# Optimization experiments

Hardware: AMD Instinct MI355X
Metric: run time of the kernel (lower is better)

## Reference

```python
import jax, jax.numpy as jnp
import numpy as np

B, S, D, H = 2, 2048, 1024, 16
HD = D // H  # head dim 64
LN_EPS = 1e-12


def setup_inputs() -> dict:
    key = jax.random.key(0)
    ks = jax.random.split(key, 10)
    sc = 0.02
    return {
        "input_tensor": jax.random.normal(ks[0], (B, S, D), dtype=jnp.float32),
        "attention_mask": jnp.zeros((B, 1, 1, S), dtype=jnp.float32),
        "Wq": jax.random.normal(ks[1], (D, D), dtype=jnp.float32) * sc,
        "bq": jnp.zeros((D,), dtype=jnp.float32),
        "Wk": jax.random.normal(ks[2], (D, D), dtype=jnp.float32) * sc,
        "bk": jnp.zeros((D,), dtype=jnp.float32),
        "Wv": jax.random.normal(ks[3], (D, D), dtype=jnp.float32) * sc,
        "bv": jnp.zeros((D,), dtype=jnp.float32),
        "Wo": jax.random.normal(ks[4], (D, D), dtype=jnp.float32) * sc,
        "bo": jnp.zeros((D,), dtype=jnp.float32),
        "ln_gamma": jnp.ones((D,), dtype=jnp.float32),
        "ln_beta": jnp.zeros((D,), dtype=jnp.float32),
    }


def _split_heads(x):
    # [B,S,D] -> [B,H,S,hd]
    return x.reshape(B, S, H, HD).transpose(0, 2, 1, 3)


def reference(input_tensor, attention_mask, Wq, bq, Wk, bk, Wv, bv, Wo, bo, ln_gamma, ln_beta):
    q = _split_heads(input_tensor @ Wq + bq)
    k = _split_heads(input_tensor @ Wk + bk)
    v = _split_heads(input_tensor @ Wv + bv)
    scores = jnp.einsum("bhqd,bhkd->bhqk", q, k) / jnp.sqrt(jnp.float32(HD))
    scores = scores + attention_mask  # additive mask broadcast
    probs = jax.nn.softmax(scores, axis=-1)
    ctx = jnp.einsum("bhqk,bhkd->bhqd", probs, v)
    ctx = ctx.transpose(0, 2, 1, 3).reshape(B, S, D)
    hidden = ctx @ Wo + bo
    x = hidden + input_tensor
    mu = jnp.mean(x, axis=-1, keepdims=True)
    var = jnp.mean(jnp.square(x - mu), axis=-1, keepdims=True)
    return (x - mu) / jnp.sqrt(var + LN_EPS) * ln_gamma + ln_beta
```

## Files before the change

kernel.cpp:

```cpp
#include <hip/hip_runtime.h>
#include <stdint.h>

#define Bb 2
#define Ss 2048
#define Dd 1024
#define Hh 16
#define HD 64
#define Mtot 4096

typedef __bf16 bf16x8 __attribute__((ext_vector_type(8)));
typedef float f32x4 __attribute__((ext_vector_type(4)));
typedef unsigned short ushort_t;

#if __has_builtin(__builtin_amdgcn_exp2f)
#define EXP2(x) __builtin_amdgcn_exp2f(x)
#else
#define EXP2(x) __expf((x) * 0.6931472f)
#endif

__device__ __forceinline__ float bf2f(ushort_t u) {
    union { uint32_t i; float f; } v;
    v.i = ((uint32_t)u) << 16;
    return v.f;
}

__device__ __forceinline__ ushort_t f2bf(float f) {
    union { float f; uint32_t i; } v;
    v.f = f;
    uint32_t u = v.i;
    u += 0x7FFFu + ((u >> 16) & 1u);
    return (ushort_t)(u >> 16);
}

__device__ __forceinline__ uint32_t fbits(float f) {
    union { float f; uint32_t i; } v; v.f = f; return v.i;
}

__device__ __forceinline__ float load_in(const void* p, size_t i, int isf32) {
    if (isf32) return ((const float*)p)[i];
    return bf2f(((const ushort_t*)p)[i]);
}

__device__ __forceinline__ void gload_lds16(const void* g, void* l) {
    __builtin_amdgcn_global_load_lds(
        (const __attribute__((address_space(1))) void*)g,
        (__attribute__((address_space(3))) void*)l, 16, 0, 0);
}

#define NVEC 525568ull
__global__ __launch_bounds__(256) void prep_k(
    const void* X, const void* mask, const void* bq, const void* bk,
    const void* bv, const void* bo, const void* g, const void* be,
    const void* Wq, const void* Wk, const void* Wv, const void* Wo,
    int* __restrict__ flag, ushort_t* __restrict__ cX,
    ushort_t* __restrict__ cMask, ushort_t* __restrict__ cB,
    ushort_t* __restrict__ wt) {
    __shared__ int sflag;
    __shared__ ushort_t tile[32][33];
    const int tid = threadIdx.x;
    {
        const int lane = tid & 63;
        if (tid < 64) {
            const ushort_t* Xu = (const ushort_t*)X;
            int local = 0;
            for (int i = lane; i < 2048; i += 64) {
                int e = (Xu[i] >> 7) & 0xFF;
                local += (e >= 0x90);
            }
            for (int off = 1; off < 64; off <<= 1) local += __shfl_xor(local, off);
            if (lane == 0) sflag = (local >= 4) ? 1 : 0;
        }
    }
    __syncthreads();
    const int f = sflag;
    if (blockIdx.x == 0 && tid == 0) *flag = f;

    if (blockIdx.x < 1024) {
        const size_t stride = 1024ull * 256ull;
        for (size_t t = (size_t)blockIdx.x * 256 + tid; t < NVEC; t += stride) {
            const void* src;
            ushort_t* dst;
            size_t v;
            if (t < 524288ull) {
                src = X; dst = cX; v = t;
            } else if (t < 524800ull) {
                src = mask; dst = cMask; v = t - 524288ull;
            } else {
                size_t j = t - 524800ull;
                int w = (int)(j >> 7);
                src = (w == 0) ? bq : (w == 1) ? bk : (w == 2) ? bv
                    : (w == 3) ? bo : (w == 4) ? g : be;
                dst = cB + w * 1024;
                v = j & 127;
            }
            if (f) {
                const float4* s4 = (const float4*)src;
                float4 a = s4[v * 2], b = s4[v * 2 + 1];
                union { ushort_t u[8]; uint4 q; } pk;
                pk.u[0] = f2bf(a.x); pk.u[1] = f2bf(a.y);
                pk.u[2] = f2bf(a.z); pk.u[3] = f2bf(a.w);
                pk.u[4] = f2bf(b.x); pk.u[5] = f2bf(b.y);
                pk.u[6] = f2bf(b.z); pk.u[7] = f2bf(b.w);
                ((uint4*)dst)[v] = pk.q;
            } else {
                ((uint4*)dst)[v] = ((const uint4*)src)[v];
            }
        }
    } else {
        int id2 = blockIdx.x - 1024;
        int z = id2 >> 10;
        int rem = id2 & 1023;
        int bx = rem & 31, by = rem >> 5;
        const void* W = (z == 0) ? Wq : (z == 1) ? Wk : (z == 2) ? Wv : Wo;
        ushort_t* T = wt + (size_t)z * Dd * Dd;
        int tx = tid & 31, ty = tid >> 5;
        int x = bx * 32 + tx;
        int y0 = by * 32;
        for (int i = 0; i < 4; i++) {
            int y = y0 + ty + i * 8;
            tile[ty + i * 8][tx] = f2bf(load_in(W, (size_t)y * Dd + x, f));
        }
        __syncthreads();
        int x2 = by * 32 + tx;
        int y20 = bx * 32;
        for (int i = 0; i < 4; i++) {
            int y = y20 + ty + i * 8;
            T[(size_t)y * Dd + x2] = tile[tx][ty + i * 8];
        }
    }
}

__global__ __launch_bounds__(256) void gemm_qkv(
    const ushort_t* __restrict__ X, const ushort_t* __restrict__ wt,
    const ushort_t* __restrict__ cB,
    ushort_t* __restrict__ Qb, ushort_t* __restrict__ Kb, ushort_t* __restrict__ Vtb) {
    const int z = blockIdx.z;
    const ushort_t* Wt = wt + (size_t)z * Dd * Dd;
    const ushort_t* bias = cB + z * 1024;

    __shared__ __align__(16) ushort_t smem[2][2][128 * 32];

    const int tid = threadIdx.x;
    const int lane = tid & 63, wv = tid >> 6;
    const int quad = lane >> 4, l15 = lane & 15;
    const int wrow = (wv >> 1) * 64, wcol = (wv & 1) * 64;
    const int row0 = blockIdx.y * 128, col0 = blockIdx.x * 128;
    const int lrow = lane >> 2, lcol = (lane & 3) * 8;

    const f32x4 fzero = {0.f, 0.f, 0.f, 0.f};
    f32x4 acc[4][4];
    for (int mt = 0; mt < 4; mt++)
        for (int nt = 0; nt < 4; nt++) acc[mt][nt] = fzero;

    for (int j = 0; j < 2; j++) {
        int ch = wv * 2 + j;
        gload_lds16(&X[(size_t)(row0 + ch * 16 + lrow) * Dd + lcol],
                    &smem[0][0][ch * 512]);
        gload_lds16(&Wt[(size_t)(col0 + ch * 16 + lrow) * Dd + lcol],
                    &smem[0][1][ch * 512]);
    }

    for (int k0 = 0; k0 < Dd; k0 += 32) {
        const int buf = (k0 >> 5) & 1;
        __syncthreads();
        if (k0 + 32 < Dd) {
            for (int j = 0; j < 2; j++) {
                int ch = wv * 2 + j;
                gload_lds16(&X[(size_t)(row0 + ch * 16 + lrow) * Dd + k0 + 32 + lcol],
                            &smem[buf ^ 1][0][ch * 512]);
                gload_lds16(&Wt[(size_t)(col0 + ch * 16 + lrow) * Dd + k0 + 32 + lcol],
                            &smem[buf ^ 1][1][ch * 512]);
            }
        }
        const ushort_t* As = &smem[buf][0][0];
        const ushort_t* Bs = &smem[buf][1][0];
        bf16x8 af[4], bfr[4];
        for (int mt = 0; mt < 4; mt++)
            af[mt] = *(const bf16x8*)(&As[(wrow + mt * 16 + l15) * 32 + quad * 8]);
        for (int nt = 0; nt < 4; nt++)
            bfr[nt] = *(const bf16x8*)(&Bs[(wcol + nt * 16 + l15) * 32 + quad * 8]);
        for (int mt = 0; mt < 4; mt++)
            for (int nt = 0; nt < 4; nt++)
                acc[mt][nt] = __builtin_amdgcn_mfma_f32_16x16x32_bf16(
                    af[mt], bfr[nt], acc[mt][nt], 0, 0, 0);
    }

    const float qscale = 0.18033688f;
    ushort_t* Cs = &smem[0][0][0];
    for (int mt = 0; mt < 4; mt++) {
        __syncthreads();
        for (int nt = 0; nt < 4; nt++) {
            int gn = col0 + wcol + nt * 16 + l15;
            float bv_ = bf2f(bias[gn]);
            for (int r = 0; r < 4; r++) {
                float v = acc[mt][nt][r] + bv_;
                if (z == 0) v *= qscale;
                int ric = (wv >> 1) * 16 + quad * 4 + r;
                Cs[ric * 136 + wcol + nt * 16 + l15] = f2bf(v);
            }
        }
        __syncthreads();
        if (z == 2) {
            int c = tid >> 1, r0 = (tid & 1) * 16;
            int gn = col0 + c, h = gn >> 6, d = gn & 63;
            int gmbase = row0 + (r0 >> 4) * 64 + mt * 16;
            int b = gmbase >> 11, s0 = gmbase & 2047;
            union { ushort_t u[16]; uint4 q[2]; } pk;
            for (int i = 0; i < 16; i++) pk.u[i] = Cs[(r0 + i) * 136 + c];
            uint4* dst = (uint4*)&Vtb[((size_t)((b * Hh + h) * HD + d)) * Ss + s0];
            dst[0] = pk.q[0];
            dst[1] = pk.q[1];
        } else {
            int ric = tid >> 3, c0 = (tid & 7) * 16;
            int gm = row0 + (ric >> 4) * 64 + mt * 16 + (ric & 15);
            int gn = col0 + c0, h = gn >> 6, d0 = gn & 63;
            int b = gm >> 11, s = gm & 2047;
            const uint4* src = (const uint4*)&Cs[ric * 136 + c0];
            ushort_t* Ob = (z == 0) ? Qb : Kb;
            uint4* dst = (uint4*)&Ob[((size_t)((b * Hh + h) * Ss + s)) * HD + d0];
            dst[0] = src[0];
            dst[1] = src[1];
        }
    }
}

#define STR 76
__global__ __launch_bounds__(512) void attn(
    const ushort_t* __restrict__ Q, const ushort_t* __restrict__ K,
    const ushort_t* __restrict__ Vt, const ushort_t* __restrict__ mask,
    ushort_t* __restrict__ ctx) {
    const int tid = threadIdx.x;
    const int lane = tid & 63, wv = tid >> 6;
    const int quad = lane >> 4, l15 = lane & 15;
    const int bh = blockIdx.x;
    const int b = bh >> 4, h = bh & 15;
    const int q0 = blockIdx.y * 128 + wv * 16;

    const ushort_t* Qh = Q + (size_t)bh * Ss * HD;
    const ushort_t* Kh = K + (size_t)bh * Ss * HD;
    const ushort_t* Vh = Vt + (size_t)bh * HD * Ss;

    __shared__ __align__(16) ushort_t Ks[2][64 * 64];
    __shared__ __align__(16) ushort_t Vs[2][64 * 64];
    __shared__ __align__(16) float maskF[Ss];
    __shared__ __align__(16) ushort_t Pl[8][16 * STR];
    ushort_t* Pw = &Pl[wv][0];

    for (int i = tid; i < Ss; i += 512)
        maskF[i] = (bf2f(mask[b * Ss + i]) - 4.0f) * 1.4426950f;

    const int r8 = lane >> 3, c8 = lane & 7, gc = c8 ^ r8;
    const int sw = l15 & 7;

    gload_lds16(&Kh[(size_t)(wv * 8 + r8) * HD + gc * 8], &Ks[0][wv * 512]);
    gload_lds16(&Vh[(size_t)(wv * 8 + r8) * Ss + gc * 8], &Vs[0][wv * 512]);

    bf16x8 qf[2];
    qf[0] = *(const bf16x8*)(&Qh[(size_t)(q0 + l15) * HD + quad * 8]);
    qf[1] = *(const bf16x8*)(&Qh[(size_t)(q0 + l15) * HD + 32 + quad * 8]);

    bf16x8 onesf;
    {
        union { ushort_t u[8]; bf16x8 v; } ou;
        for (int i = 0; i < 8; i++) ou.u[i] = 0x3F80;
        onesf = ou.v;
    }

    const f32x4 fzero = {0.f, 0.f, 0.f, 0.f};
    f32x4 o[4];
    for (int dt = 0; dt < 4; dt++) o[dt] = fzero;
    f32x4 o_l = fzero;

    for (int kb = 0; kb < Ss; kb += 64) {
        const int buf = (kb >> 6) & 1;
        __syncthreads();

        if (kb + 64 < Ss) {
            gload_lds16(&Kh[(size_t)(kb + 64 + wv * 8 + r8) * HD + gc * 8],
                        &Ks[buf ^ 1][wv * 512]);
            gload_lds16(&Vh[(size_t)(wv * 8 + r8) * Ss + kb + 64 + gc * 8],
                        &Vs[buf ^ 1][wv * 512]);
        }

        const ushort_t* ks = &Ks[buf][0];
        const ushort_t* vs = &Vs[buf][0];

        f32x4 st[4];
        for (int kt = 0; kt < 4; kt++) {
            f32x4 mk = *(const f32x4*)(&maskF[kb + kt * 16 + quad * 4]);
            bf16x8 kf0 = *(const bf16x8*)(&ks[(kt * 16 + l15) * 64 + ((quad) ^ sw) * 8]);
            bf16x8 kf1 = *(const bf16x8*)(&ks[(kt * 16 + l15) * 64 + ((quad + 4) ^ sw) * 8]);
            st[kt] = __builtin_amdgcn_mfma_f32_16x16x32_bf16(kf0, qf[0], mk, 0, 0, 0);
            st[kt] = __builtin_amdgcn_mfma_f32_16x16x32_bf16(kf1, qf[1], st[kt], 0, 0, 0);
        }

        for (int kt = 0; kt < 4; kt++) {
            float e0 = EXP2(st[kt][0]);
            float e1 = EXP2(st[kt][1]);
            float e2 = EXP2(st[kt][2]);
            float e3 = EXP2(st[kt][3]);
            uint2 pk;
            pk.x = __builtin_amdgcn_perm(fbits(e1), fbits(e0), 0x07060302u);
            pk.y = __builtin_amdgcn_perm(fbits(e3), fbits(e2), 0x07060302u);
            *(uint2*)(&Pw[l15 * STR + kt * 16 + quad * 4]) = pk;
        }

        for (int c = 0; c < 2; c++) {
            union { uint2 u2[2]; bf16x8 v; } pu;
            pu.u2[0] = *(const uint2*)(&Pw[l15 * STR + c * 32 + quad * 8]);
            pu.u2[1] = *(const uint2*)(&Pw[l15 * STR + c * 32 + quad * 8 + 4]);
            bf16x8 pf = pu.v;
            for (int dt = 0; dt < 4; dt++) {
                bf16x8 vf = *(const bf16x8*)(
                    &vs[(dt * 16 + l15) * 64 + ((c * 4 + quad) ^ sw) * 8]);
                o[dt] = __builtin_amdgcn_mfma_f32_16x16x32_bf16(pf, vf, o[dt], 0, 0, 0);
            }
            o_l = __builtin_amdgcn_mfma_f32_16x16x32_bf16(pf, onesf, o_l, 0, 0, 0);
        }
    }

    for (int r = 0; r < 4; r++) {
        int q = q0 + quad * 4 + r;
        float linv = 1.f / o_l[r];
        for (int dt = 0; dt < 4; dt++) {
            ctx[((size_t)(b * Ss + q)) * Dd + h * HD + dt * 16 + l15] =
                f2bf(o[dt][r] * linv);
        }
    }
}

__global__ __launch_bounds__(256) void gemm_out(
    const ushort_t* __restrict__ A, const ushort_t* __restrict__ Wt,
    const ushort_t* __restrict__ bo, const ushort_t* __restrict__ X,
    ushort_t* __restrict__ xout) {
    __shared__ __align__(16) ushort_t smem[2][6144];

    const int tid = threadIdx.x;
    const int lane = tid & 63, wv = tid >> 6;
    const int quad = lane >> 4, l15 = lane & 15;
    const int wrow = (wv >> 1) * 32, wcol = (wv & 1) * 64;
    const int row0 = blockIdx.y * 64, col0 = blockIdx.x * 128;
    const int lrow = lane >> 2, lcol = (lane & 3) * 8;

    const f32x4 fzero = {0.f, 0.f, 0.f, 0.f};
    f32x4 acc[2][4];
    for (int mt = 0; mt < 2; mt++)
        for (int nt = 0; nt < 4; nt++) acc[mt][nt] = fzero;

    gload_lds16(&A[(size_t)(row0 + wv * 16 + lrow) * Dd + lcol], &smem[0][wv * 512]);
    for (int j = 0; j < 2; j++) {
        int ch = wv * 2 + j;
        gload_lds16(&Wt[(size_t)(col0 + ch * 16 + lrow) * Dd + lcol],
                    &smem[0][2048 + ch * 512]);
    }

    for (int k0 = 0; k0 < Dd; k0 += 32) {
        const int buf = (k0 >> 5) & 1;
        __syncthreads();
        if (k0 + 32 < Dd) {
            gload_lds16(&A[(size_t)(row0 + wv * 16 + lrow) * Dd + k0 + 32 + lcol],
                        &smem[buf ^ 1][wv * 512]);
            for (int j = 0; j < 2; j++) {
                int ch = wv * 2 + j;
                gload_lds16(&Wt[(size_t)(col0 + ch * 16 + lrow) * Dd + k0 + 32 + lcol],
                            &smem[buf ^ 1][2048 + ch * 512]);
            }
        }
        const ushort_t* As = &smem[buf][0];
        const ushort_t* Bs = &smem[buf][2048];
        bf16x8 af[2], bfr[4];
        for (int mt = 0; mt < 2; mt++)
            af[mt] = *(const bf16x8*)(&As[(wrow + mt * 16 + l15) * 32 + quad * 8]);
        for (int nt = 0; nt < 4; nt++)
            bfr[nt] = *(const bf16x8*)(&Bs[(wcol + nt * 16 + l15) * 32 + quad * 8]);
        for (int mt = 0; mt < 2; mt++)
            for (int nt = 0; nt < 4; nt++)
                acc[mt][nt] = __builtin_amdgcn_mfma_f32_16x16x32_bf16(
                    af[mt], bfr[nt], acc[mt][nt], 0, 0, 0);
    }

    for (int mt = 0; mt < 2; mt++)
        for (int nt = 0; nt < 4; nt++)
            for (int r = 0; r < 4; r++) {
                int gm = row0 + wrow + mt * 16 + quad * 4 + r;
                int gn = col0 + wcol + nt * 16 + l15;
                float v = acc[mt][nt][r] + bf2f(bo[gn]) + bf2f(X[(size_t)gm * Dd + gn]);
                xout[(size_t)gm * Dd + gn] = f2bf(v);
            }
}

__global__ __launch_bounds__(256) void ln_k(
    const ushort_t* __restrict__ x, const ushort_t* __restrict__ gamma,
    const ushort_t* __restrict__ beta, const int* __restrict__ flag,
    void* __restrict__ out) {
    const int row = blockIdx.x;
    const int tid = threadIdx.x;
    const int f = *flag;

    union { uint2 q; ushort_t u[4]; } xv;
    xv.q = ((const uint2*)(x + (size_t)row * Dd))[tid];
    float xi[4];
    for (int i = 0; i < 4; i++) xi[i] = bf2f(xv.u[i]);
    float s = (xi[0] + xi[1]) + (xi[2] + xi[3]);
    float ss = (xi[0] * xi[0] + xi[1] * xi[1]) + (xi[2] * xi[2] + xi[3] * xi[3]);
    for (int off = 1; off < 64; off <<= 1) {
        s += __shfl_xor(s, off);
        ss += __shfl_xor(ss, off);
    }
    __shared__ float ps[4], pss[4];
    int wv = tid >> 6;
    if ((tid & 63) == 0) { ps[wv] = s; pss[wv] = ss; }
    __syncthreads();
    s = ps[0] + ps[1] + ps[2] + ps[3];
    ss = pss[0] + pss[1] + pss[2] + pss[3];
    float mu = s * (1.f / Dd);
    float var = ss * (1.f / Dd) - mu * mu;
    float rstd = rsqrtf(fmaxf(var, 0.f) + 1e-12f);

    const int c0 = tid * 4;
    float r[4];
    for (int i = 0; i < 4; i++) {
        float g = bf2f(gamma[c0 + i]);
        float bb = bf2f(beta[c0 + i]);
        r[i] = (xi[i] - mu) * rstd * g + bb;
    }
    if (f) {
        float4 o4 = {r[0], r[1], r[2], r[3]};
        ((float4*)out)[(size_t)row * 256 + tid] = o4;
    } else {
        union { ushort_t u[4]; uint2 q; } pk;
        for (int i = 0; i < 4; i++) pk.u[i] = f2bf(r[i]);
        *(uint2*)((ushort_t*)out + (size_t)row * Dd + c0) = pk.q;
    }
}

extern "C" void kernel_launch(void* const* d_in, const int* in_sizes, int n_in,
                              void* d_out, int out_size, void* d_ws, size_t ws_size,
                              hipStream_t stream) {
    char* ws = (char*)d_ws;
    int* flag       = (int*)ws;
    ushort_t* cMask = (ushort_t*)(ws + (64ull << 10));
    ushort_t* cB    = (ushort_t*)(ws + (96ull << 10));
    ushort_t* cX    = (ushort_t*)(ws + (1ull << 20));
    ushort_t* wt    = (ushort_t*)(ws + (17ull << 20));
    ushort_t* Qb    = (ushort_t*)(ws + (25ull << 20));
    ushort_t* Kb    = (ushort_t*)(ws + (33ull << 20));
    ushort_t* Vtb   = (ushort_t*)(ws + (41ull << 20));
    ushort_t* ctx   = (ushort_t*)(ws + (49ull << 20));
    ushort_t* xbuf  = (ushort_t*)(ws + (25ull << 20));

    hipLaunchKernelGGL(prep_k, dim3(5120), dim3(256), 0, stream,
                       d_in[0], d_in[1], d_in[3], d_in[5], d_in[7], d_in[9],
                       d_in[10], d_in[11], d_in[2], d_in[4], d_in[6], d_in[8],
                       flag, cX, cMask, cB, wt);
    hipLaunchKernelGGL(gemm_qkv, dim3(8, 32, 3), dim3(256), 0, stream,
                       cX, wt, cB, Qb, Kb, Vtb);
    hipLaunchKernelGGL(attn, dim3(32, 16), dim3(512), 0, stream,
                       Qb, Kb, Vtb, cMask, ctx);
    hipLaunchKernelGGL(gemm_out, dim3(8, 64), dim3(256), 0, stream,
                       ctx, wt + 3ull * Dd * Dd, cB + 3 * 1024, cX, xbuf);
    hipLaunchKernelGGL(ln_k, dim3(Mtot), dim3(256), 0, stream,
                       xbuf, cB + 4 * 1024, cB + 5 * 1024, flag, d_out);
}
```

Baseline: 210.1 us.

## Switch attention to 32x32x16 MFMA with register-resident P via permlane32 swap

Rewrites the attention kernel to use 32x32x16 bf16 MFMA tiles, with 4 waves each handling 32 query rows instead of 8 waves of 16. The softmax probabilities are converted with v_cvt_pk_bf16_f32 and rearranged in registers with v_permlane32_swap instead of round-tripping through an LDS P buffer. It also adds s_setprio around the MFMA sections and sets launch bounds to 256 threads with 2 blocks per CU. The aim is to cut LDS traffic and instruction overhead per FLOP, at the cost of higher register pressure from the 16-wide accumulators.

```diff
diff --git a/kernel.cpp b/kernel.cpp
--- a/kernel.cpp
+++ b/kernel.cpp
@@ -10,6 +10,7 @@
 
 typedef __bf16 bf16x8 __attribute__((ext_vector_type(8)));
 typedef float f32x4 __attribute__((ext_vector_type(4)));
+typedef float f32x16 __attribute__((ext_vector_type(16)));
 typedef unsigned short ushort_t;
 
 #if __has_builtin(__builtin_amdgcn_exp2f)
@@ -32,8 +33,10 @@
     return (ushort_t)(u >> 16);
 }
 
-__device__ __forceinline__ uint32_t fbits(float f) {
-    union { float f; uint32_t i; } v; v.f = f; return v.i;
+__device__ __forceinline__ uint32_t cvtpk_bf16(float lo, float hi) {
+    uint32_t r;
+    asm("v_cvt_pk_bf16_f32 %0, %1, %2" : "=v"(r) : "v"(lo), "v"(hi));
+    return r;
 }
 
 __device__ __forceinline__ float load_in(const void* p, size_t i, int isf32) {
@@ -224,17 +227,16 @@
     }
 }
 
-#define STR 76
-__global__ __launch_bounds__(512) void attn(
+__global__ __launch_bounds__(256, 2) void attn(
     const ushort_t* __restrict__ Q, const ushort_t* __restrict__ K,
     const ushort_t* __restrict__ Vt, const ushort_t* __restrict__ mask,
     ushort_t* __restrict__ ctx) {
     const int tid = threadIdx.x;
     const int lane = tid & 63, wv = tid >> 6;
-    const int quad = lane >> 4, l15 = lane & 15;
+    const int n = lane & 31, hi = lane >> 5;
     const int bh = blockIdx.x;
     const int b = bh >> 4, h = bh & 15;
-    const int q0 = blockIdx.y * 128 + wv * 16;
+    const int q0 = blockIdx.y * 128 + wv * 32;
 
     const ushort_t* Qh = Q + (size_t)bh * Ss * HD;
     const ushort_t* Kh = K + (size_t)bh * Ss * HD;
@@ -243,21 +245,23 @@
     __shared__ __align__(16) ushort_t Ks[2][64 * 64];
     __shared__ __align__(16) ushort_t Vs[2][64 * 64];
     __shared__ __align__(16) float maskF[Ss];
-    __shared__ __align__(16) ushort_t Pl[8][16 * STR];
-    ushort_t* Pw = &Pl[wv][0];
-
-    for (int i = tid; i < Ss; i += 512)
+
+    for (int i = tid; i < Ss; i += 256)
         maskF[i] = (bf2f(mask[b * Ss + i]) - 4.0f) * 1.4426950f;
 
     const int r8 = lane >> 3, c8 = lane & 7, gc = c8 ^ r8;
-    const int sw = l15 & 7;
-
-    gload_lds16(&Kh[(size_t)(wv * 8 + r8) * HD + gc * 8], &Ks[0][wv * 512]);
-    gload_lds16(&Vh[(size_t)(wv * 8 + r8) * Ss + gc * 8], &Vs[0][wv * 512]);
-
-    bf16x8 qf[2];
-    qf[0] = *(const bf16x8*)(&Qh[(size_t)(q0 + l15) * HD + quad * 8]);
-    qf[1] = *(const bf16x8*)(&Qh[(size_t)(q0 + l15) * HD + 32 + quad * 8]);
+    const int sw = n & 7;
+
+    for (int j = 0; j < 2; j++) {
+        int row = wv * 16 + j * 8;
+        gload_lds16(&Kh[(size_t)(row + r8) * HD + gc * 8], &Ks[0][row * 64]);
+        gload_lds16(&Vh[(size_t)(row + r8) * Ss + gc * 8], &Vs[0][row * 64]);
+    }
+
+    bf16x8 qf[4];
+#pragma unroll
+    for (int ks = 0; ks < 4; ks++)
+        qf[ks] = *(const bf16x8*)(&Qh[(size_t)(q0 + n) * HD + ks * 16 + hi * 8]);
 
     bf16x8 onesf;
     {
@@ -266,64 +270,89 @@
         onesf = ou.v;
     }
 
-    const f32x4 fzero = {0.f, 0.f, 0.f, 0.f};
-    f32x4 o[4];
-    for (int dt = 0; dt < 4; dt++) o[dt] = fzero;
-    f32x4 o_l = fzero;
+    f32x16 o[2], o_l;
+#pragma unroll
+    for (int r = 0; r < 16; r++) { o[0][r] = 0.f; o[1][r] = 0.f; o_l[r] = 0.f; }
 
     for (int kb = 0; kb < Ss; kb += 64) {
         const int buf = (kb >> 6) & 1;
         __syncthreads();
 
         if (kb + 64 < Ss) {
-            gload_lds16(&Kh[(size_t)(kb + 64 + wv * 8 + r8) * HD + gc * 8],
-                        &Ks[buf ^ 1][wv * 512]);
-            gload_lds16(&Vh[(size_t)(wv * 8 + r8) * Ss + kb + 64 + gc * 8],
-                        &Vs[buf ^ 1][wv * 512]);
-        }
-
-        const ushort_t* ks = &Ks[buf][0];
-        const ushort_t* vs = &Vs[buf][0];
-
-        f32x4 st[4];
-        for (int kt = 0; kt < 4; kt++) {
-            f32x4 mk = *(const f32x4*)(&maskF[kb + kt * 16 + quad * 4]);
-            bf16x8 kf0 = *(const bf16x8*)(&ks[(kt * 16 + l15) * 64 + ((quad) ^ sw) * 8]);
-            bf16x8 kf1 = *(const bf16x8*)(&ks[(kt * 16 + l15) * 64 + ((quad + 4) ^ sw) * 8]);
-            st[kt] = __builtin_amdgcn_mfma_f32_16x16x32_bf16(kf0, qf[0], mk, 0, 0, 0);
-            st[kt] = __builtin_amdgcn_mfma_f32_16x16x32_bf16(kf1, qf[1], st[kt], 0, 0, 0);
-        }
-
-        for (int kt = 0; kt < 4; kt++) {
-            float e0 = EXP2(st[kt][0]);
-            float e1 = EXP2(st[kt][1]);
-            float e2 = EXP2(st[kt][2]);
-            float e3 = EXP2(st[kt][3]);
-            uint2 pk;
-            pk.x = __builtin_amdgcn_perm(fbits(e1), fbits(e0), 0x07060302u);
-            pk.y = __builtin_amdgcn_perm(fbits(e3), fbits(e2), 0x07060302u);
-            *(uint2*)(&Pw[l15 * STR + kt * 16 + quad * 4]) = pk;
-        }
-
-        for (int c = 0; c < 2; c++) {
-            union { uint2 u2[2]; bf16x8 v; } pu;
-            pu.u2[0] = *(const uint2*)(&Pw[l15 * STR + c * 32 + quad * 8]);
-            pu.u2[1] = *(const uint2*)(&Pw[l15 * STR + c * 32 + quad * 8 + 4]);
-            bf16x8 pf = pu.v;
-            for (int dt = 0; dt < 4; dt++) {
+            for (int j = 0; j < 2; j++) {
+                int row = wv * 16 + j * 8;
+                gload_lds16(&Kh[(size_t)(kb + 64 + row + r8) * HD + gc * 8],
+                            &Ks[buf ^ 1][row * 64]);
+                gload_lds16(&Vh[(size_t)(row + r8) * Ss + kb + 64 + gc * 8],
+                            &Vs[buf ^ 1][row * 64]);
+            }
+        }
+
+        const ushort_t* ks_ = &Ks[buf][0];
+        const ushort_t* vs_ = &Vs[buf][0];
+
+        f32x16 st[2];
+#pragma unroll
+        for (int mt = 0; mt < 2; mt++) {
+#pragma unroll
+            for (int r4 = 0; r4 < 4; r4++) {
+                f32x4 mk = *(const f32x4*)(&maskF[kb + mt * 32 + r4 * 8 + hi * 4]);
+                st[mt][r4 * 4 + 0] = mk[0];
+                st[mt][r4 * 4 + 1] = mk[1];
+                st[mt][r4 * 4 + 2] = mk[2];
+                st[mt][r4 * 4 + 3] = mk[3];
+            }
+        }
+        __builtin_amdgcn_s_setprio(1);
+#pragma unroll
+        for (int mt = 0; mt < 2; mt++) {
+#pragma unroll
+            for (int ksp = 0; ksp < 4; ksp++) {
+                bf16x8 kf = *(const bf16x8*)(
+                    &ks_[(mt * 32 + n) * 64 + ((ksp * 2 + hi) ^ sw) * 8]);
+                st[mt] = __builtin_amdgcn_mfma_f32_32x32x16_bf16(
+                    kf, qf[ksp], st[mt], 0, 0, 0);
+            }
+        }
+        __builtin_amdgcn_s_setprio(0);
+
+#pragma unroll
+        for (int mt = 0; mt < 2; mt++)
+#pragma unroll
+            for (int r = 0; r < 16; r++) st[mt][r] = EXP2(st[mt][r]);
+
+#pragma unroll
+        for (int c = 0; c < 4; c++) {
+            const int mt = c >> 1, cc = (c & 1) * 8;
+            uint32_t a0 = cvtpk_bf16(st[mt][cc + 0], st[mt][cc + 1]);
+            uint32_t a1 = cvtpk_bf16(st[mt][cc + 2], st[mt][cc + 3]);
+            uint32_t b0 = cvtpk_bf16(st[mt][cc + 4], st[mt][cc + 5]);
+            uint32_t b1 = cvtpk_bf16(st[mt][cc + 6], st[mt][cc + 7]);
+            asm("v_permlane32_swap_b32 %0, %1" : "+v"(a0), "+v"(b0));
+            asm("v_permlane32_swap_b32 %0, %1" : "+v"(a1), "+v"(b1));
+            union { uint32_t w[4]; bf16x8 v; } pa;
+            pa.w[0] = a0; pa.w[1] = a1; pa.w[2] = b0; pa.w[3] = b1;
+            __builtin_amdgcn_s_setprio(1);
+#pragma unroll
+            for (int dt = 0; dt < 2; dt++) {
                 bf16x8 vf = *(const bf16x8*)(
-                    &vs[(dt * 16 + l15) * 64 + ((c * 4 + quad) ^ sw) * 8]);
-                o[dt] = __builtin_amdgcn_mfma_f32_16x16x32_bf16(pf, vf, o[dt], 0, 0, 0);
-            }
-            o_l = __builtin_amdgcn_mfma_f32_16x16x32_bf16(pf, onesf, o_l, 0, 0, 0);
-        }
-    }
-
-    for (int r = 0; r < 4; r++) {
-        int q = q0 + quad * 4 + r;
+                    &vs_[(dt * 32 + n) * 64 + ((c * 2 + hi) ^ sw) * 8]);
+                o[dt] = __builtin_amdgcn_mfma_f32_32x32x16_bf16(
+                    pa.v, vf, o[dt], 0, 0, 0);
+            }
+            o_l = __builtin_amdgcn_mfma_f32_32x32x16_bf16(
+                pa.v, onesf, o_l, 0, 0, 0);
+            __builtin_amdgcn_s_setprio(0);
+        }
+    }
+
+#pragma unroll
+    for (int r = 0; r < 16; r++) {
+        int q = q0 + (r & 3) + 8 * (r >> 2) + 4 * hi;
         float linv = 1.f / o_l[r];
-        for (int dt = 0; dt < 4; dt++) {
-            ctx[((size_t)(b * Ss + q)) * Dd + h * HD + dt * 16 + l15] =
+#pragma unroll
+        for (int dt = 0; dt < 2; dt++) {
+            ctx[((size_t)(b * Ss + q)) * Dd + h * HD + dt * 32 + n] =
                 f2bf(o[dt][r] * linv);
         }
     }
@@ -455,7 +484,7 @@
                        flag, cX, cMask, cB, wt);
     hipLaunchKernelGGL(gemm_qkv, dim3(8, 32, 3), dim3(256), 0, stream,
                        cX, wt, cB, Qb, Kb, Vtb);
-    hipLaunchKernelGGL(attn, dim3(32, 16), dim3(512), 0, stream,
+    hipLaunchKernelGGL(attn, dim3(32, 16), dim3(256), 0, stream,
                        Qb, Kb, Vtb, cMask, ctx);
     hipLaunchKernelGGL(gemm_out, dim3(8, 64), dim3(256), 0, stream,
                        ctx, wt + 3ull * Dd * Dd, cB + 3 * 1024, cX, xbuf);
```

After: 205.0 us. 2.4% less time.
